# Performance work log

Hardware: AMD Instinct MI355X
Metric: run time of the kernel (lower is better)

The kernel has to match this reference:

```python
import jax, jax.numpy as jnp
import numpy as np

G = 5      # kan_grid: number of grid intervals on [-1, 1]
K = 3      # kan_k: B-spline order

def make_grid(in_dim, dtype=jnp.float32):
    # pykan extended grid: uniform on [-1,1] with G intervals, extended by K knots each side
    h = 2.0 / G
    pts = jnp.arange(-K, G + K + 1, dtype=dtype) * h - 1.0   # (G + 2K + 1,)
    return jnp.broadcast_to(pts, (in_dim, G + 2 * K + 1))

def b_spline_basis(x, grid):
    # x: (N, D), grid: (D, M).  Cox-de Boor recursion, vectorized over (N, D).
    xe = x[:, :, None]                      # (N, D, 1)
    g = grid[None, :, :]                    # (1, D, M)
    B = ((xe >= g[:, :, :-1]) & (xe < g[:, :, 1:])).astype(x.dtype)  # order 0
    for p in range(1, K + 1):
        B = ((xe - g[:, :, :-(p + 1)]) / (g[:, :, p:-1] - g[:, :, :-(p + 1)])) * B[:, :, :-1] \
          + ((g[:, :, p + 1:] - xe) / (g[:, :, p + 1:] - g[:, :, 1:-p])) * B[:, :, 1:]
    return B                                # (N, D, G + K)

def kan_layer(x, coef, scale_base, scale_sp):
    # pykan KANLayer: out_o = sum_i [ sb[i,o]*silu(x_i) + ss[i,o]*sum_g B(x_i)_g * coef[i,o,g] ]
    in_dim = x.shape[1]
    B = b_spline_basis(x, make_grid(in_dim, x.dtype))          # (N, D, G+K)
    y_base = jnp.einsum('ni,io->no', jax.nn.silu(x), scale_base)
    y_sp = jnp.einsum('nig,iog,io->no', B, coef, scale_sp)
    return y_base + y_sp

def setup_inputs() -> dict:
    key = jax.random.key(0)
    ks = jax.random.split(key, 5)
    d_model, hidden = 512, 1024
    bsz, seq = 4, 1024
    ncoef = G + K
    x = jax.random.normal(ks[0], (bsz, seq, d_model), dtype=jnp.float32)
    coef1 = 0.1 * jax.random.normal(ks[1], (d_model, hidden, ncoef), dtype=jnp.float32)
    coef2 = 0.1 * jax.random.normal(ks[2], (hidden, d_model, ncoef), dtype=jnp.float32)
    scale_base1 = (1.0 / np.sqrt(d_model)) * jax.random.normal(ks[3], (d_model, hidden), dtype=jnp.float32)
    scale_base2 = (1.0 / np.sqrt(hidden)) * jax.random.normal(ks[4], (hidden, d_model), dtype=jnp.float32)
    scale_sp1 = jnp.ones((d_model, hidden), dtype=jnp.float32)
    scale_sp2 = jnp.ones((hidden, d_model), dtype=jnp.float32)
    return {"x": x, "coef1": coef1, "scale_base1": scale_base1, "scale_sp1": scale_sp1,
            "coef2": coef2, "scale_base2": scale_base2, "scale_sp2": scale_sp2}

def reference(x, coef1, scale_base1, scale_sp1, coef2, scale_base2, scale_sp2):
    bsz, seq, d_model = x.shape
    flat = x.reshape(-1, d_model)                      # (N, d_model); chunking is math-neutral
    h = kan_layer(flat, coef1, scale_base1, scale_sp1)  # (N, hidden)
    out = kan_layer(h, coef2, scale_base2, scale_sp2)   # (N, d_model)
    return out.reshape(bsz, seq, d_model)              # dropout p=0.0 -> identity
```

## Files before the change

### kernel.cpp

```cpp
#include <hip/hip_runtime.h>
#include <hip/hip_bf16.h>
#include <cstdint>
#include <cstddef>

typedef float  f32x4 __attribute__((ext_vector_type(4)));
typedef _Float16 f16x8 __attribute__((ext_vector_type(8)));
typedef _Float16 f16x4 __attribute__((ext_vector_type(4)));

#define DEVFN __device__ __forceinline__

DEVFN void bspline8(float x, float bv[8]) {
    float t[12];
#pragma unroll
    for (int j = 0; j < 12; ++j) t[j] = (float)(j - 3) * 0.4f - 1.0f;
    float B[11];
#pragma unroll
    for (int j = 0; j < 11; ++j) B[j] = (x >= t[j] && x < t[j + 1]) ? 1.0f : 0.0f;
    const float rp[3] = {2.5f, 1.25f, 0.8333333333f};
#pragma unroll
    for (int p = 1; p <= 3; ++p) {
#pragma unroll
        for (int j = 0; j + p < 11; ++j) {
            float left  = (x - t[j]) * rp[p - 1];
            float right = (t[j + p + 1] - x) * rp[p - 1];
            B[j] = left * B[j] + right * B[j + 1];
        }
    }
#pragma unroll
    for (int g = 0; g < 8; ++g) bv[g] = B[g];
}

DEVFN float silu_f(float x) {
    return x * __builtin_amdgcn_rcpf(1.0f + __expf(-x));
}

__global__ void prep_a_kernel(const float* __restrict__ X,
                              _Float16* __restrict__ Aaug,
                              int total4, int dshift) {
    int idx = blockIdx.x * 256 + threadIdx.x;
    if (idx >= total4) return;
    const int D  = 1 << dshift;
    const int K  = 9 << dshift;
    const int dq = dshift - 2;
    const int n  = idx >> dq;
    const int i4 = (idx & ((1 << dq) - 1)) << 2;
    f32x4 x = *(const f32x4*)(X + (size_t)n * D + i4);
    float bv[4][8];
    f16x4 v;
#pragma unroll
    for (int e = 0; e < 4; ++e) {
        v[e] = (_Float16)silu_f(x[e]);
        bspline8(x[e], bv[e]);
    }
    _Float16* dst = Aaug + (size_t)n * K + i4;
    *(f16x4*)dst = v;
#pragma unroll
    for (int g = 0; g < 8; ++g) {
        f16x4 u;
#pragma unroll
        for (int e = 0; e < 4; ++e) u[e] = (_Float16)bv[e][g];
        *(f16x4*)(dst + (size_t)(g + 1) * D) = u;
    }
}

__global__ void prep_a_red_kernel(const float* __restrict__ HP,
                                  _Float16* __restrict__ Aaug,
                                  int total4, int dshift, size_t pstride) {
    int idx = blockIdx.x * 256 + threadIdx.x;
    if (idx >= total4) return;
    const int D  = 1 << dshift;
    const int K  = 9 << dshift;
    const int dq = dshift - 2;
    const int n  = idx >> dq;
    const int i4 = (idx & ((1 << dq) - 1)) << 2;
    const size_t off = (size_t)n * D + i4;
    f32x4 x = (*(const f32x4*)(HP + off) + *(const f32x4*)(HP + off + pstride)) +
              (*(const f32x4*)(HP + off + 2 * pstride) +
               *(const f32x4*)(HP + off + 3 * pstride));
    float bv[4][8];
    f16x4 v;
#pragma unroll
    for (int e = 0; e < 4; ++e) {
        v[e] = (_Float16)silu_f(x[e]);
        bspline8(x[e], bv[e]);
    }
    _Float16* dst = Aaug + (size_t)n * K + i4;
    *(f16x4*)dst = v;
#pragma unroll
    for (int g = 0; g < 8; ++g) {
        f16x4 u;
#pragma unroll
        for (int e = 0; e < 4; ++e) u[e] = (_Float16)bv[e][g];
        *(f16x4*)(dst + (size_t)(g + 1) * D) = u;
    }
}

__global__ void reduce_out_kernel(const float* __restrict__ OP,
                                  float* __restrict__ out,
                                  int total4, size_t pstride4) {
    int i = blockIdx.x * 256 + threadIdx.x;
    if (i >= total4) return;
    const f32x4* p = (const f32x4*)OP;
    f32x4 s = p[i];
#pragma unroll
    for (int k = 1; k < 8; ++k) s += p[i + k * pstride4];
    ((f32x4*)out)[i] = s;
}

__global__ void prep_w_kernel(const float* __restrict__ coef,
                              const float* __restrict__ sb,
                              const float* __restrict__ sp,
                              _Float16* __restrict__ WT,
                              int total, int din_shift, int dout) {
    int idx = blockIdx.x * 256 + threadIdx.x;
    if (idx >= total) return;
    const int Din = 1 << din_shift;
    const int i = idx & (Din - 1);
    const int o = idx >> din_shift;
    const size_t K = (size_t)9 << din_shift;
    const size_t cidx = (size_t)i * dout + o;
    float base  = sb[cidx];
    float scale = sp[cidx];
    const float* cp = coef + cidx * 8;
    _Float16* dst = WT + (size_t)o * K + i;
    dst[0] = (_Float16)base;
#pragma unroll
    for (int g = 0; g < 8; ++g) dst[(size_t)(g + 1) * Din] = (_Float16)(cp[g] * scale);
}

DEVFN void gload16(const void* g, void* l) {
    __builtin_amdgcn_global_load_lds(
        (const __attribute__((address_space(1))) void*)g,
        (__attribute__((address_space(3))) void*)l, 16, 0, 0);
}

__global__ __launch_bounds__(512, 2) void gemm256_f16_bt(
    const _Float16* __restrict__ A,
    const _Float16* __restrict__ WT,
    float* __restrict__ P,
    int K, int N, int klen, int gxshift) {
    constexpr int BK = 64;
    __shared__ _Float16 Alds[2][256 * BK];
    __shared__ _Float16 Blds[2][256 * BK];

    const int tid  = threadIdx.x;
    const int lane = tid & 63;
    const int w    = tid >> 6;
    const int wm   = w >> 2;
    const int wn   = w & 3;

    const int gx   = 1 << gxshift;
    const int nwg  = gx * 16 * gridDim.z;
    const int orig = blockIdx.x + (blockIdx.y << gxshift) + blockIdx.z * (gx * 16);
    const int tile = (orig & 7) * (nwg >> 3) + (orig >> 3);
    const int col  = tile & (gx - 1);
    const int rs   = tile >> gxshift;
    const int row  = rs & 15;
    const int spl  = rs >> 4;

    const size_t bm = (size_t)row * 256;
    const size_t bn = (size_t)col * 256;
    const int kbase = spl * klen;
    const int nt    = klen / BK;
    float* Cp = P + (size_t)spl * 4096 * N;

    const f32x4 vzero = {0.0f, 0.0f, 0.0f, 0.0f};
    f32x4 acc[8][4];
#pragma unroll
    for (int m = 0; m < 8; ++m)
#pragma unroll
        for (int n = 0; n < 4; ++n) acc[m][n] = vzero;

    const int srow = tid >> 3;
    const int c8   = tid & 7;
    const int ldst = w * 512;
    const int l15  = lane & 15;
    const int gk   = lane >> 4;

#define STAGE(b, kk)                                                         \
    {                                                                        \
        _Pragma("unroll")                                                    \
        for (int is = 0; is < 4; ++is) {                                     \
            const int r  = is * 64 + srow;                                   \
            const int sg = (c8 ^ (r & 7)) << 3;                              \
            gload16(A + (bm + r) * (size_t)K + (kk) + sg,                    \
                    &Alds[b][is * 4096 + ldst]);                             \
            gload16(WT + (bn + r) * (size_t)K + (kk) + sg,                   \
                    &Blds[b][is * 4096 + ldst]);                             \
        }                                                                    \
    }

#define AADDR(buf, r2, ks2) \
    (&Alds[buf][(r2) * BK + (((((ks2) * 4) + gk) ^ ((r2) & 7)) << 3)])
#define BADDR(buf, r2, ks2) \
    (&Blds[buf][(r2) * BK + (((((ks2) * 4) + gk) ^ ((r2) & 7)) << 3)])

    STAGE(0, kbase);

    for (int t = 0; t < nt; ++t) {
        const int cur = t & 1;
        if (t + 1 < nt) {
            STAGE(cur ^ 1, kbase + (t + 1) * BK);
            asm volatile("s_waitcnt vmcnt(8)" ::: "memory");
        } else {
            asm volatile("s_waitcnt vmcnt(0)" ::: "memory");
        }
        __builtin_amdgcn_s_barrier();
        __builtin_amdgcn_sched_barrier(0);

        f16x8 af[4][2], bf0[2][2], bf1[2][2];

#pragma unroll
        for (int m = 0; m < 4; ++m)
#pragma unroll
            for (int ks = 0; ks < 2; ++ks) {
                const int r2 = wm * 128 + m * 16 + l15;
                af[m][ks] = *(const f16x8*)AADDR(cur, r2, ks);
            }
#pragma unroll
        for (int n = 0; n < 2; ++n)
#pragma unroll
            for (int ks = 0; ks < 2; ++ks) {
                const int r2 = wn * 64 + n * 16 + l15;
                bf0[n][ks] = *(const f16x8*)BADDR(cur, r2, ks);
            }
        __builtin_amdgcn_s_setprio(1);
#pragma unroll
        for (int m = 0; m < 4; ++m)
#pragma unroll
            for (int n = 0; n < 2; ++n)
#pragma unroll
                for (int ks = 0; ks < 2; ++ks)
                    acc[m][n] = __builtin_amdgcn_mfma_f32_16x16x32_f16(
                        af[m][ks], bf0[n][ks], acc[m][n], 0, 0, 0);
        __builtin_amdgcn_s_setprio(0);
        __builtin_amdgcn_s_barrier();
        __builtin_amdgcn_sched_barrier(0);

#pragma unroll
        for (int n = 0; n < 2; ++n)
#pragma unroll
            for (int ks = 0; ks < 2; ++ks) {
                const int r2 = wn * 64 + 32 + n * 16 + l15;
                bf1[n][ks] = *(const f16x8*)BADDR(cur, r2, ks);
            }
        __builtin_amdgcn_s_setprio(1);
#pragma unroll
        for (int m = 0; m < 4; ++m)
#pragma unroll
            for (int n = 0; n < 2; ++n)
#pragma unroll
                for (int ks = 0; ks < 2; ++ks)
                    acc[m][n + 2] = __builtin_amdgcn_mfma_f32_16x16x32_f16(
                        af[m][ks], bf1[n][ks], acc[m][n + 2], 0, 0, 0);
        __builtin_amdgcn_s_setprio(0);
        __builtin_amdgcn_s_barrier();
        __builtin_amdgcn_sched_barrier(0);

#pragma unroll
        for (int m = 0; m < 4; ++m)
#pragma unroll
            for (int ks = 0; ks < 2; ++ks) {
                const int r2 = wm * 128 + 64 + m * 16 + l15;
                af[m][ks] = *(const f16x8*)AADDR(cur, r2, ks);
            }
        __builtin_amdgcn_s_setprio(1);
#pragma unroll
        for (int m = 0; m < 4; ++m)
#pragma unroll
            for (int n = 0; n < 2; ++n)
#pragma unroll
                for (int ks = 0; ks < 2; ++ks)
                    acc[m + 4][n + 2] = __builtin_amdgcn_mfma_f32_16x16x32_f16(
                        af[m][ks], bf1[n][ks], acc[m + 4][n + 2], 0, 0, 0);
        __builtin_amdgcn_s_setprio(0);
        __builtin_amdgcn_s_barrier();
        __builtin_amdgcn_sched_barrier(0);

        __builtin_amdgcn_s_setprio(1);
#pragma unroll
        for (int m = 0; m < 4; ++m)
#pragma unroll
            for (int n = 0; n < 2; ++n)
#pragma unroll
                for (int ks = 0; ks < 2; ++ks)
                    acc[m + 4][n] = __builtin_amdgcn_mfma_f32_16x16x32_f16(
                        af[m][ks], bf0[n][ks], acc[m + 4][n], 0, 0, 0);
        __builtin_amdgcn_s_setprio(0);
        __builtin_amdgcn_s_barrier();
        __builtin_amdgcn_sched_barrier(0);
    }
#undef STAGE
#undef AADDR
#undef BADDR

    const int r0 = wm * 128 + (lane >> 4) * 4;
    const int c0 = wn * 64 + (lane & 15);
#pragma unroll
    for (int m = 0; m < 8; ++m)
#pragma unroll
        for (int n = 0; n < 4; ++n)
#pragma unroll
            for (int r = 0; r < 4; ++r)
                Cp[(bm + r0 + m * 16 + r) * (size_t)N + bn + c0 + n * 16] =
                    acc[m][n][r];
}

extern "C" void kernel_launch(void* const* d_in, const int* in_sizes, int n_in,
                              void* d_out, int out_size, void* d_ws, size_t ws_size,
                              hipStream_t stream) {
    const float* x     = (const float*)d_in[0];
    const float* coef1 = (const float*)d_in[1];
    const float* sb1   = (const float*)d_in[2];
    const float* sp1   = (const float*)d_in[3];
    const float* coef2 = (const float*)d_in[4];
    const float* sb2   = (const float*)d_in[5];
    const float* sp2   = (const float*)d_in[6];
    float* out = (float*)d_out;

    const int M  = 4096;
    const int D1 = 512;
    const int D2 = 1024;
    const int K1 = 9 * D1;
    const int K2 = 9 * D2;

    char* ws = (char*)d_ws;
    _Float16* Aaug = (_Float16*)ws;
    _Float16* WT   = (_Float16*)(ws + (size_t)M * K2 * 2);
    float*    P    = (float*)(ws + (size_t)M * K2 * 2 +
                              (size_t)D1 * K2 * 2);

    prep_w_kernel<<<(D1 * D2) / 256, 256, 0, stream>>>(coef1, sb1, sp1, WT,
                                                       D1 * D2, 9, D2);
    prep_a_kernel<<<(M * D1 / 4) / 256, 256, 0, stream>>>(x, Aaug, M * D1 / 4, 9);
    {
        dim3 grid(D2 / 256, M / 256, 4);
        gemm256_f16_bt<<<grid, 512, 0, stream>>>(Aaug, WT, P, K1, D2, K1 / 4, 2);
    }
    prep_w_kernel<<<(D2 * D1) / 256, 256, 0, stream>>>(coef2, sb2, sp2, WT,
                                                       D1 * D2, 10, D1);
    prep_a_red_kernel<<<(M * D2 / 4) / 256, 256, 0, stream>>>(
        P, Aaug, M * D2 / 4, 10, (size_t)M * D2);
    {
        dim3 grid(D1 / 256, M / 256, 8);
        gemm256_f16_bt<<<grid, 512, 0, stream>>>(Aaug, WT, P, K2, D1, K2 / 8, 1);
    }
    reduce_out_kernel<<<(M * D1 / 4) / 256, 256, 0, stream>>>(
        P, out, M * D1 / 4, (size_t)M * D1 / 4);
}
```

Baseline: 257.1 us.

## Switch GEMM mainloop to 4-slot BK=32 pipeline with three stages in flight

Replaces the double-buffered BK=64 main loop with a four-slot ring of BK=32 K-slices. Three slices are kept in flight through global_load_lds, with graded vmcnt waits as the loop drains. Each slice loads all A and B fragments at once and issues 32 MFMAs between just two barriers, instead of four interleaved sub-phases. This aims to hide more global-load latency and cut barrier count per FLOP, but each iteration now holds 12 fragments in registers and the LDS swizzle is changed to match the 32-wide rows.

```diff
diff --git a/kernel.cpp b/kernel.cpp
--- a/kernel.cpp
+++ b/kernel.cpp
@@ -139,9 +139,8 @@
     const _Float16* __restrict__ WT,
     float* __restrict__ P,
     int K, int N, int klen, int gxshift) {
-    constexpr int BK = 64;
-    __shared__ _Float16 Alds[2][256 * BK];
-    __shared__ _Float16 Blds[2][256 * BK];
+    __shared__ _Float16 Alds[4][8192];
+    __shared__ _Float16 Blds[4][8192];
 
     const int tid  = threadIdx.x;
     const int lane = tid & 63;
@@ -161,7 +160,7 @@
     const size_t bm = (size_t)row * 256;
     const size_t bn = (size_t)col * 256;
     const int kbase = spl * klen;
-    const int nt    = klen / BK;
+    const int NP    = klen >> 5;
     float* Cp = P + (size_t)spl * 4096 * N;
 
     const f32x4 vzero = {0.0f, 0.0f, 0.0f, 0.0f};
@@ -171,128 +170,73 @@
 #pragma unroll
         for (int n = 0; n < 4; ++n) acc[m][n] = vzero;
 
-    const int srow = tid >> 3;
-    const int c8   = tid & 7;
+    const int srow = tid >> 2;
+    const int scg  = tid & 3;
     const int ldst = w * 512;
     const int l15  = lane & 15;
-    const int gk   = lane >> 4;
-
-#define STAGE(b, kk)                                                         \
+    const int gk2  = lane >> 4;
+
+#define ISSUE(u)                                                             \
     {                                                                        \
+        const int slot_ = (u) & 3;                                           \
+        const int kq_   = kbase + (((u) >> 1) << 6) + (((u) & 1) << 5);      \
         _Pragma("unroll")                                                    \
-        for (int is = 0; is < 4; ++is) {                                     \
-            const int r  = is * 64 + srow;                                   \
-            const int sg = (c8 ^ (r & 7)) << 3;                              \
-            gload16(A + (bm + r) * (size_t)K + (kk) + sg,                    \
-                    &Alds[b][is * 4096 + ldst]);                             \
-            gload16(WT + (bn + r) * (size_t)K + (kk) + sg,                   \
-                    &Blds[b][is * 4096 + ldst]);                             \
+        for (int is = 0; is < 2; ++is) {                                     \
+            const int r_  = is * 128 + srow;                                 \
+            const int sg_ = (scg ^ ((r_ >> 1) & 3)) << 3;                    \
+            gload16(A + (bm + r_) * (size_t)K + kq_ + sg_,                   \
+                    &Alds[slot_][is * 4096 + ldst]);                         \
+            gload16(WT + (bn + r_) * (size_t)K + kq_ + sg_,                  \
+                    &Blds[slot_][is * 4096 + ldst]);                         \
         }                                                                    \
     }
 
-#define AADDR(buf, r2, ks2) \
-    (&Alds[buf][(r2) * BK + (((((ks2) * 4) + gk) ^ ((r2) & 7)) << 3)])
-#define BADDR(buf, r2, ks2) \
-    (&Blds[buf][(r2) * BK + (((((ks2) * 4) + gk) ^ ((r2) & 7)) << 3)])
-
-    STAGE(0, kbase);
-
-    for (int t = 0; t < nt; ++t) {
-        const int cur = t & 1;
-        if (t + 1 < nt) {
-            STAGE(cur ^ 1, kbase + (t + 1) * BK);
+#define FROFF(r2) (((r2) * 32) + (((gk2 ^ (((r2) >> 1) & 3))) << 3))
+
+    ISSUE(0);
+    ISSUE(1);
+    ISSUE(2);
+
+    for (int p = 0; p < NP; ++p) {
+        const int slot  = p & 3;
+        const int ahead = NP - 1 - p;
+        if (ahead >= 3) {
+            ISSUE(p + 3);
+            asm volatile("s_waitcnt vmcnt(12)" ::: "memory");
+        } else if (ahead == 2) {
             asm volatile("s_waitcnt vmcnt(8)" ::: "memory");
+        } else if (ahead == 1) {
+            asm volatile("s_waitcnt vmcnt(4)" ::: "memory");
         } else {
             asm volatile("s_waitcnt vmcnt(0)" ::: "memory");
         }
         __builtin_amdgcn_s_barrier();
         __builtin_amdgcn_sched_barrier(0);
 
-        f16x8 af[4][2], bf0[2][2], bf1[2][2];
-
-#pragma unroll
-        for (int m = 0; m < 4; ++m)
-#pragma unroll
-            for (int ks = 0; ks < 2; ++ks) {
-                const int r2 = wm * 128 + m * 16 + l15;
-                af[m][ks] = *(const f16x8*)AADDR(cur, r2, ks);
-            }
-#pragma unroll
-        for (int n = 0; n < 2; ++n)
-#pragma unroll
-            for (int ks = 0; ks < 2; ++ks) {
-                const int r2 = wn * 64 + n * 16 + l15;
-                bf0[n][ks] = *(const f16x8*)BADDR(cur, r2, ks);
-            }
+        f16x8 af[8], bf[4];
+#pragma unroll
+        for (int m = 0; m < 8; ++m) {
+            const int r2 = wm * 128 + m * 16 + l15;
+            af[m] = *(const f16x8*)(&Alds[slot][FROFF(r2)]);
+        }
+#pragma unroll
+        for (int n = 0; n < 4; ++n) {
+            const int r2 = wn * 64 + n * 16 + l15;
+            bf[n] = *(const f16x8*)(&Blds[slot][FROFF(r2)]);
+        }
         __builtin_amdgcn_s_setprio(1);
 #pragma unroll
-        for (int m = 0; m < 4; ++m)
-#pragma unroll
-            for (int n = 0; n < 2; ++n)
-#pragma unroll
-                for (int ks = 0; ks < 2; ++ks)
-                    acc[m][n] = __builtin_amdgcn_mfma_f32_16x16x32_f16(
-                        af[m][ks], bf0[n][ks], acc[m][n], 0, 0, 0);
+        for (int m = 0; m < 8; ++m)
+#pragma unroll
+            for (int n = 0; n < 4; ++n)
+                acc[m][n] = __builtin_amdgcn_mfma_f32_16x16x32_f16(
+                    af[m], bf[n], acc[m][n], 0, 0, 0);
         __builtin_amdgcn_s_setprio(0);
         __builtin_amdgcn_s_barrier();
         __builtin_amdgcn_sched_barrier(0);
-
-#pragma unroll
-        for (int n = 0; n < 2; ++n)
-#pragma unroll
-            for (int ks = 0; ks < 2; ++ks) {
-                const int r2 = wn * 64 + 32 + n * 16 + l15;
-                bf1[n][ks] = *(const f16x8*)BADDR(cur, r2, ks);
-            }
-        __builtin_amdgcn_s_setprio(1);
-#pragma unroll
-        for (int m = 0; m < 4; ++m)
-#pragma unroll
-            for (int n = 0; n < 2; ++n)
-#pragma unroll
-                for (int ks = 0; ks < 2; ++ks)
-                    acc[m][n + 2] = __builtin_amdgcn_mfma_f32_16x16x32_f16(
-                        af[m][ks], bf1[n][ks], acc[m][n + 2], 0, 0, 0);
-        __builtin_amdgcn_s_setprio(0);
-        __builtin_amdgcn_s_barrier();
-        __builtin_amdgcn_sched_barrier(0);
-
-#pragma unroll
-        for (int m = 0; m < 4; ++m)
-#pragma unroll
-            for (int ks = 0; ks < 2; ++ks) {
-                const int r2 = wm * 128 + 64 + m * 16 + l15;
-                af[m][ks] = *(const f16x8*)AADDR(cur, r2, ks);
-            }
-        __builtin_amdgcn_s_setprio(1);
-#pragma unroll
-        for (int m = 0; m < 4; ++m)
-#pragma unroll
-            for (int n = 0; n < 2; ++n)
-#pragma unroll
-                for (int ks = 0; ks < 2; ++ks)
-                    acc[m + 4][n + 2] = __builtin_amdgcn_mfma_f32_16x16x32_f16(
-                        af[m][ks], bf1[n][ks], acc[m + 4][n + 2], 0, 0, 0);
-        __builtin_amdgcn_s_setprio(0);
-        __builtin_amdgcn_s_barrier();
-        __builtin_amdgcn_sched_barrier(0);
-
-        __builtin_amdgcn_s_setprio(1);
-#pragma unroll
-        for (int m = 0; m < 4; ++m)
-#pragma unroll
-            for (int n = 0; n < 2; ++n)
-#pragma unroll
-                for (int ks = 0; ks < 2; ++ks)
-                    acc[m + 4][n] = __builtin_amdgcn_mfma_f32_16x16x32_f16(
-                        af[m][ks], bf0[n][ks], acc[m + 4][n], 0, 0, 0);
-        __builtin_amdgcn_s_setprio(0);
-        __builtin_amdgcn_s_barrier();
-        __builtin_amdgcn_sched_barrier(0);
-    }
-#undef STAGE
-#undef AADDR
-#undef BADDR
+    }
+#undef ISSUE
+#undef FROFF
 
     const int r0 = wm * 128 + (lane >> 4) * 4;
     const int c0 = wn * 64 + (lane & 15);
```

Result: slower. 264.1 us (+2.7%).
